# Kernel optimization log

Hardware: AMD Instinct MI355X
Metric: run time of the kernel (lower is better)

Reference implementation:

```python
import jax, jax.numpy as jnp
import numpy as np

L, B, F, H, C = 1024, 8, 256, 8, 32  # seq, batch, feature_dim, heads, head_size
EPS = 1e-5


def setup_inputs() -> dict:
    key = jax.random.key(0)
    ks = jax.random.split(key, 12)
    s = 0.02
    f32 = jnp.float32
    return {
        "features": jax.random.normal(ks[0], (L, B, F), f32),
        "ln_g": jnp.ones((F,), f32),
        "ln_b": jnp.zeros((F,), f32),
        "Wq": jax.random.normal(ks[1], (F, H * C), f32) * s,
        "bq": jnp.zeros((H * C,), f32),
        "Wk": jax.random.normal(ks[2], (F, H * C), f32) * s,
        "bk": jnp.zeros((H * C,), f32),
        "Wv": jax.random.normal(ks[3], (F, H * C), f32) * s,
        "bv": jnp.zeros((H * C,), f32),
        "Wb": jax.random.normal(ks[4], (F, H), f32) * s,
        "bb": jnp.zeros((H,), f32),
        "Wg": jax.random.normal(ks[5], (F, H * C), f32) * s,
        "bg": jnp.zeros((H * C,), f32),
        "Wo": jax.random.normal(ks[6], (H * C, F), f32) * s,
        "bo": jnp.zeros((F,), f32),
    }


def _layernorm(x, g, b):
    mu = jnp.mean(x, axis=-1, keepdims=True)
    var = jnp.var(x, axis=-1, keepdims=True)
    return (x - mu) * jax.lax.rsqrt(var + EPS) * g + b


def reference(features, ln_g, ln_b, Wq, bq, Wk, bk, Wv, bv, Wb, bb, Wg, bg, Wo, bo):
    # features: (L, B, F) -- sequence-first layout (see einsum axis analysis)
    x = _layernorm(features, ln_g, ln_b)
    q = (x @ Wq + bq).reshape(L, B, H, C)  # (Lq, B, H, C)
    k = (x @ Wk + bk).reshape(L, B, H, C)  # (Lk, B, H, C)
    v = (x @ Wv + bv).reshape(L, B, H, C)
    bias = x @ Wb + bb                      # (Lk, B, H) per-key-position bias
    gate = jax.nn.sigmoid(x @ Wg + bg).reshape(L, B, H, C)

    sq_c = 1.0 / np.sqrt(C).astype(np.float32)
    # logits[q, b, k, h]
    logits = jnp.einsum('qbhc,kbhc->qbkh', q, k) * sq_c
    logits = logits + jnp.transpose(bias, (1, 0, 2))[None]  # (1, B, Lk, H)
    w = jax.nn.softmax(logits, axis=2)                      # softmax over keys
    attn = jnp.einsum('qbkh,kbhc->qbhc', w, v)              # (Lq, B, H, C)
    out = (attn * gate).reshape(L, B, H * C)
    return out @ Wo + bo                                    # (L, B, F)
```

## Files before the change

kernel.cpp:

```cpp
#include <hip/hip_runtime.h>
#include <math.h>

#define LQ 1024
#define BB 8
#define FF 256
#define HH 8
#define CC 32
#define MROWS (LQ*BB)
static constexpr float EPSV  = 1e-5f;
static constexpr float LOG2E = 1.4426950408889634f;
static constexpr float C1    = 0.17677669529663687f * 1.4426950408889634f;

typedef short  short8  __attribute__((ext_vector_type(8)));
typedef short  short4v __attribute__((ext_vector_type(4)));
typedef float  float4v __attribute__((ext_vector_type(4)));

__device__ inline unsigned short f2bf(float f) {
    unsigned int u = __builtin_bit_cast(unsigned int, f);
    u += 0x7FFFu + ((u >> 16) & 1u);
    return (unsigned short)(u >> 16);
}
__device__ inline float bf2f(unsigned short h) {
    unsigned int u = ((unsigned int)h) << 16;
    return __builtin_bit_cast(float, u);
}
__device__ inline unsigned int cvt_pk_bf16(float a, float b) {
    unsigned int r;
    asm("v_cvt_pk_bf16_f32 %0, %1, %2" : "=v"(r) : "v"(a), "v"(b));
    return r;
}
__device__ __forceinline__ void gl_lds16(const unsigned short* g, unsigned short* l) {
    __builtin_amdgcn_global_load_lds(
        (const __attribute__((address_space(1))) void*)g,
        (__attribute__((address_space(3))) void*)l, 16, 0, 0);
}

__global__ __launch_bounds__(256)
void prep_ln_kernel(const float* __restrict__ x, const float* __restrict__ g,
                    const float* __restrict__ bln,
                    const float* __restrict__ Wq, const float* __restrict__ Wk,
                    const float* __restrict__ Wv, const float* __restrict__ Wg,
                    const float* __restrict__ Wo, const float* __restrict__ Wb,
                    const float* __restrict__ bq, const float* __restrict__ bk,
                    const float* __restrict__ bv, const float* __restrict__ bg,
                    unsigned short* __restrict__ xb, unsigned short* __restrict__ wt,
                    unsigned short* __restrict__ wto,
                    float* __restrict__ bcomb, float* __restrict__ wbt) {
    int bid = blockIdx.x;
    if (bid < 2048) {
        int wid  = threadIdx.x >> 6;
        int lane = threadIdx.x & 63;
        int row  = bid * 4 + wid;
        float4 v = reinterpret_cast<const float4*>(x + (size_t)row * FF)[lane];
        float s  = v.x + v.y + v.z + v.w;
        float sq = v.x*v.x + v.y*v.y + v.z*v.z + v.w*v.w;
        #pragma unroll
        for (int m = 1; m < 64; m <<= 1) {
            s  += __shfl_xor(s,  m);
            sq += __shfl_xor(sq, m);
        }
        float mean = s * (1.0f / FF);
        float var  = sq * (1.0f / FF) - mean * mean;
        float rstd = rsqrtf(var + EPSV);
        float4 gg = reinterpret_cast<const float4*>(g)[lane];
        float4 bv4 = reinterpret_cast<const float4*>(bln)[lane];
        short4v o;
        o[0] = (short)f2bf((v.x - mean) * rstd * gg.x + bv4.x);
        o[1] = (short)f2bf((v.y - mean) * rstd * gg.y + bv4.y);
        o[2] = (short)f2bf((v.z - mean) * rstd * gg.z + bv4.z);
        o[3] = (short)f2bf((v.w - mean) * rstd * gg.w + bv4.w);
        *reinterpret_cast<short4v*>(xb + (size_t)row * FF + lane * 4) = o;
    } else if (bid < 2112) {
        int k0 = (bid - 2048) * 4;
        int nl = threadIdx.x;
        const float* Ws[5] = {Wq, Wk, Wv, Wg, Wo};
        #pragma unroll
        for (int sel = 0; sel < 5; ++sel) {
            const float* W = Ws[sel];
            short4v o;
            #pragma unroll
            for (int j = 0; j < 4; ++j)
                o[j] = (short)f2bf(W[(size_t)(k0 + j) * 256 + nl]);
            unsigned short* dst = (sel < 4)
                ? (wt + ((size_t)sel * 256 + nl) * 256 + k0)
                : (wto + (size_t)nl * 256 + k0);
            *reinterpret_cast<short4v*>(dst) = o;
        }
        if (k0 == 0) {
            bcomb[nl]       = bq[nl];
            bcomb[256 + nl] = bk[nl];
            bcomb[512 + nl] = bv[nl];
            bcomb[768 + nl] = bg[nl];
        }
    } else {
        int nl = threadIdx.x;
        #pragma unroll
        for (int hh = 0; hh < 8; ++hh)
            wbt[hh * 256 + nl] = Wb[(size_t)nl * 8 + hh];
    }
}

__global__ __launch_bounds__(256)
void qkvg_fused_kernel(const unsigned short* __restrict__ A,
                       const unsigned short* __restrict__ Bt,
                       const float* __restrict__ bcomb,
                       const float* __restrict__ wbt,
                       const float* __restrict__ bbv,
                       unsigned short* __restrict__ outq,
                       float* __restrict__ outb) {
    __shared__ unsigned short Asb[128 * 64];
    __shared__ unsigned short Bsb[128 * 64];
    int bid = blockIdx.x;
    int tid = threadIdx.x;

    if (bid >= 512) {
        int idx = (bid - 512) * 256 + tid;
        int row = idx >> 3, hh = idx & 7;
        const unsigned short* xr = A + (size_t)row * 256;
        const float* wr = wbt + hh * 256;
        float s = 0.f;
        #pragma unroll 4
        for (int i = 0; i < 32; ++i) {
            short8 x8 = *reinterpret_cast<const short8*>(xr + i * 8);
            float4 wa = *reinterpret_cast<const float4*>(wr + i * 8);
            float4 wb2 = *reinterpret_cast<const float4*>(wr + i * 8 + 4);
            s += bf2f((unsigned short)x8[0]) * wa.x + bf2f((unsigned short)x8[1]) * wa.y
               + bf2f((unsigned short)x8[2]) * wa.z + bf2f((unsigned short)x8[3]) * wa.w;
            s += bf2f((unsigned short)x8[4]) * wb2.x + bf2f((unsigned short)x8[5]) * wb2.y
               + bf2f((unsigned short)x8[6]) * wb2.z + bf2f((unsigned short)x8[7]) * wb2.w;
        }
        outb[idx] = s + bbv[hh];
        return;
    }

    int lane = tid & 63;
    int w    = tid >> 6;
    int wm   = w >> 1, wn = w & 1;
    int l15  = lane & 15, lg = lane >> 4;
    int bm   = (bid & 63) * 128;
    int bn   = (bid >> 6) * 128;

    float4v acc[4][4];
    #pragma unroll
    for (int i = 0; i < 4; ++i)
        #pragma unroll
        for (int j = 0; j < 4; ++j)
            acc[i][j] = (float4v){0.f, 0.f, 0.f, 0.f};

    for (int k0 = 0; k0 < 256; k0 += 64) {
        __syncthreads();
        #pragma unroll
        for (int j = 0; j < 4; ++j) {
            int c = w * 4 + j;
            int u = c * 64 + lane;
            int row = u >> 3, slot = u & 7;
            size_t gsw = (size_t)row * 256 + k0 + ((slot ^ (row & 7)) * 8);
            gl_lds16(A + (size_t)bm * 256 + gsw, Asb + c * 512);
            gl_lds16(Bt + (size_t)bn * 256 + gsw, Bsb + c * 512);
        }
        __syncthreads();
        #pragma unroll
        for (int kh = 0; kh < 2; ++kh) {
            int slot = kh * 4 + lg;
            short8 af[4], bf[4];
            #pragma unroll
            for (int mf = 0; mf < 4; ++mf) {
                int row = wm * 64 + mf * 16 + l15;
                af[mf] = *reinterpret_cast<const short8*>(
                    Asb + row * 64 + ((slot ^ (row & 7)) * 8));
            }
            #pragma unroll
            for (int nf = 0; nf < 4; ++nf) {
                int row = wn * 64 + nf * 16 + l15;
                bf[nf] = *reinterpret_cast<const short8*>(
                    Bsb + row * 64 + ((slot ^ (row & 7)) * 8));
            }
            #pragma unroll
            for (int mf = 0; mf < 4; ++mf)
                #pragma unroll
                for (int nf = 0; nf < 4; ++nf)
                    acc[mf][nf] = __builtin_amdgcn_mfma_f32_16x16x32_bf16(
                        bf[nf], af[mf], acc[mf][nf], 0, 0, 0);
        }
    }

    int sel = bn >> 8;
    unsigned short* outp = outq + (size_t)sel * MROWS * 256;
    #pragma unroll
    for (int mf = 0; mf < 4; ++mf) {
        int m = bm + wm * 64 + mf * 16 + l15;
        #pragma unroll
        for (int nf = 0; nf < 4; ++nf) {
            int nglob = bn + wn * 64 + nf * 16 + lg * 4;
            float4 b4 = *reinterpret_cast<const float4*>(bcomb + nglob);
            float v0 = acc[mf][nf][0] + b4.x;
            float v1 = acc[mf][nf][1] + b4.y;
            float v2 = acc[mf][nf][2] + b4.z;
            float v3 = acc[mf][nf][3] + b4.w;
            if (sel == 3) {
                v0 = 1.0f / (1.0f + __expf(-v0));
                v1 = 1.0f / (1.0f + __expf(-v1));
                v2 = 1.0f / (1.0f + __expf(-v2));
                v3 = 1.0f / (1.0f + __expf(-v3));
            }
            uint2 st;
            st.x = cvt_pk_bf16(v0, v1);
            st.y = cvt_pk_bf16(v2, v3);
            *reinterpret_cast<uint2*>(outp + (size_t)m * 256 + (nglob & 255)) = st;
        }
    }
}

__global__ __launch_bounds__(512)
void attn_mfma_kernel(const unsigned short* __restrict__ qkvg,
                      const float* __restrict__ biasp,
                      unsigned short* __restrict__ ag) {
    __shared__ unsigned short ksl[128][40];
    __shared__ unsigned short vt[32 * 128];
    __shared__ unsigned short ps[8][32 * 64];
    __shared__ float bias_s[128];
    const unsigned short* qb = qkvg;
    const unsigned short* kb = qkvg + (size_t)MROWS * 256;
    const unsigned short* vb = qkvg + (size_t)MROWS * 256 * 2;
    const unsigned short* gb = qkvg + (size_t)MROWS * 256 * 3;

    int tid  = threadIdx.x;
    int lane = tid & 63;
    int w    = tid >> 6;
    int l15  = lane & 15, lg = lane >> 4;
    int bh   = blockIdx.y;
    int b    = bh >> 3, h = bh & 7;
    int qg   = w >> 1;
    int kh2  = w & 1;
    int qrow0 = blockIdx.x * 128 + qg * 32;

    int krow = tid >> 2, kc8 = (tid & 3) * 8;
    int cv = (tid & 7) * 4, kp = tid >> 3;

    short8 qf[2];
    #pragma unroll
    for (int qt = 0; qt < 2; ++qt)
        qf[qt] = *reinterpret_cast<const short8*>(
            qb + ((size_t)(qrow0 + qt * 16 + l15) * 8 + b) * 256 + h * 32 + lg * 8);

    float lsum[2] = {0.f, 0.f};
    float4v oacc[2][2];
    #pragma unroll
    for (int i = 0; i < 2; ++i)
        #pragma unroll
        for (int j = 0; j < 2; ++j) oacc[i][j] = (float4v){0.f, 0.f, 0.f, 0.f};

    short8 kreg; short4v v0r, v1r; float breg = 0.f;
    {
        kreg = *reinterpret_cast<const short8*>(
            kb + ((size_t)krow * 8 + b) * 256 + h * 32 + kc8);
        const unsigned short* vp =
            vb + ((size_t)(2 * kp) * 8 + b) * 256 + h * 32 + cv;
        v0r = *reinterpret_cast<const short4v*>(vp);
        v1r = *reinterpret_cast<const short4v*>(vp + 8 * 256);
        if (tid < 128) breg = biasp[(size_t)tid * 64 + b * 8 + h] * LOG2E;
    }

    for (int c0 = 0; c0 < LQ; c0 += 128) {
        __syncthreads();
        *reinterpret_cast<short8*>(&ksl[krow][kc8]) = kreg;
        #pragma unroll
        for (int j = 0; j < 4; ++j) {
            int c = cv + j;
            unsigned int pk = (unsigned int)(unsigned short)v0r[j] |
                              ((unsigned int)(unsigned short)v1r[j] << 16);
            int slot = kp >> 2;
            int off  = c * 128 + ((slot ^ (c & 7)) * 8) + ((2 * kp) & 7);
            *reinterpret_cast<unsigned int*>(&vt[off]) = pk;
        }
        if (tid < 128) bias_s[tid] = breg;
        __syncthreads();
        int cn = c0 + 128;
        if (cn < LQ) {
            kreg = *reinterpret_cast<const short8*>(
                kb + ((size_t)(cn + krow) * 8 + b) * 256 + h * 32 + kc8);
            const unsigned short* vp =
                vb + ((size_t)(cn + 2 * kp) * 8 + b) * 256 + h * 32 + cv;
            v0r = *reinterpret_cast<const short4v*>(vp);
            v1r = *reinterpret_cast<const short4v*>(vp + 8 * 256);
            if (tid < 128) breg = biasp[(size_t)(cn + tid) * 64 + b * 8 + h] * LOG2E;
        }

        __builtin_amdgcn_s_setprio(1);
        float4v sc[2][4];
        #pragma unroll
        for (int kt = 0; kt < 4; ++kt) {
            short8 kf = *reinterpret_cast<const short8*>(
                &ksl[kh2 * 64 + kt * 16 + l15][lg * 8]);
            #pragma unroll
            for (int qt = 0; qt < 2; ++qt)
                sc[qt][kt] = __builtin_amdgcn_mfma_f32_16x16x32_bf16(
                    kf, qf[qt], (float4v){0.f, 0.f, 0.f, 0.f}, 0, 0, 0);
        }
        __builtin_amdgcn_s_setprio(0);

        #pragma unroll
        for (int qt = 0; qt < 2; ++qt) {
            int prow = qt * 16 + l15;
            unsigned short* pw = &ps[w][prow * 64];
            int rsw = prow & 7;
            float psum = 0.f;
            #pragma unroll
            for (int kt = 0; kt < 4; ++kt) {
                float4v b4 = *reinterpret_cast<const float4v*>(
                    &bias_s[kh2 * 64 + kt * 16 + lg * 4]);
                float p0 = __builtin_amdgcn_exp2f(fmaf(sc[qt][kt][0], C1, b4[0]));
                float p1 = __builtin_amdgcn_exp2f(fmaf(sc[qt][kt][1], C1, b4[1]));
                float p2 = __builtin_amdgcn_exp2f(fmaf(sc[qt][kt][2], C1, b4[2]));
                float p3 = __builtin_amdgcn_exp2f(fmaf(sc[qt][kt][3], C1, b4[3]));
                psum += (p0 + p1) + (p2 + p3);
                uint2 pk;
                pk.x = cvt_pk_bf16(p0, p1);
                pk.y = cvt_pk_bf16(p2, p3);
                int slot = kt * 2 + (lg >> 1);
                *reinterpret_cast<uint2*>(
                    &pw[((slot ^ rsw) * 8) + (lg & 1) * 4]) = pk;
            }
            psum += __shfl_xor(psum, 16);
            psum += __shfl_xor(psum, 32);
            lsum[qt] += psum;
        }

        __builtin_amdgcn_s_setprio(1);
        #pragma unroll
        for (int kh = 0; kh < 2; ++kh) {
            int pslot = kh * 4 + lg;
            int vslot = kh2 * 8 + kh * 4 + lg;
            short8 pf[2], vf[2];
            #pragma unroll
            for (int qt = 0; qt < 2; ++qt) {
                int prow = qt * 16 + l15;
                pf[qt] = *reinterpret_cast<const short8*>(
                    &ps[w][prow * 64 + ((pslot ^ (prow & 7)) * 8)]);
            }
            #pragma unroll
            for (int ct = 0; ct < 2; ++ct) {
                int crow = ct * 16 + l15;
                vf[ct] = *reinterpret_cast<const short8*>(
                    &vt[crow * 128 + ((vslot ^ (crow & 7)) * 8)]);
            }
            #pragma unroll
            for (int qt = 0; qt < 2; ++qt)
                #pragma unroll
                for (int ct = 0; ct < 2; ++ct)
                    oacc[qt][ct] = __builtin_amdgcn_mfma_f32_16x16x32_bf16(
                        vf[ct], pf[qt], oacc[qt][ct], 0, 0, 0);
        }
        __builtin_amdgcn_s_setprio(0);
    }

    __syncthreads();
    float* scr = reinterpret_cast<float*>(&ps[0][0]);
    if (kh2) {
        float* dst = scr + ((size_t)(qg * 64 + lane)) * 18;
        #pragma unroll
        for (int qt = 0; qt < 2; ++qt)
            #pragma unroll
            for (int ct = 0; ct < 2; ++ct)
                #pragma unroll
                for (int r = 0; r < 4; ++r)
                    dst[(qt * 2 + ct) * 4 + r] = oacc[qt][ct][r];
        dst[16] = lsum[0];
        dst[17] = lsum[1];
    }
    __syncthreads();
    if (!kh2) {
        const float* src = scr + ((size_t)(qg * 64 + lane)) * 18;
        #pragma unroll
        for (int qt = 0; qt < 2; ++qt)
            #pragma unroll
            for (int ct = 0; ct < 2; ++ct)
                #pragma unroll
                for (int r = 0; r < 4; ++r)
                    oacc[qt][ct][r] += src[(qt * 2 + ct) * 4 + r];
        lsum[0] += src[16];
        lsum[1] += src[17];

        #pragma unroll
        for (int qt = 0; qt < 2; ++qt) {
            float linv = 1.0f / lsum[qt];
            size_t base = ((size_t)(qrow0 + qt * 16 + l15) * 8 + b) * 256 + h * 32;
            #pragma unroll
            for (int ct = 0; ct < 2; ++ct) {
                int cc0 = ct * 16 + lg * 4;
                short4v g4 = *reinterpret_cast<const short4v*>(gb + base + cc0);
                float v0 = oacc[qt][ct][0] * linv * bf2f((unsigned short)g4[0]);
                float v1 = oacc[qt][ct][1] * linv * bf2f((unsigned short)g4[1]);
                float v2 = oacc[qt][ct][2] * linv * bf2f((unsigned short)g4[2]);
                float v3 = oacc[qt][ct][3] * linv * bf2f((unsigned short)g4[3]);
                uint2 st;
                st.x = cvt_pk_bf16(v0, v1);
                st.y = cvt_pk_bf16(v2, v3);
                *reinterpret_cast<uint2*>(ag + base + cc0) = st;
            }
        }
    }
}

__global__ __launch_bounds__(256)
void gemm_out_kernel(const unsigned short* __restrict__ A,
                     const unsigned short* __restrict__ Bt,
                     const float* __restrict__ bias,
                     float* __restrict__ Cout) {
    __shared__ unsigned short Asb[64 * 64];
    __shared__ unsigned short Bsb[64 * 64];
    int tid  = threadIdx.x;
    int lane = tid & 63;
    int w    = tid >> 6;
    int l15  = lane & 15, lg = lane >> 4;
    int bm   = blockIdx.x * 64;
    int bn   = blockIdx.y * 64;

    float4v acc[4];
    #pragma unroll
    for (int i = 0; i < 4; ++i) acc[i] = (float4v){0.f, 0.f, 0.f, 0.f};

    for (int k0 = 0; k0 < 256; k0 += 64) {
        __syncthreads();
        #pragma unroll
        for (int j = 0; j < 2; ++j) {
            int c = w * 2 + j;
            int u = c * 64 + lane;
            int row = u >> 3, slot = u & 7;
            gl_lds16(A + (size_t)(bm + row) * 256 + k0 + ((slot ^ (row & 7)) * 8),
                     Asb + c * 512);
        }
        #pragma unroll
        for (int j = 0; j < 2; ++j) {
            int c = w * 2 + j;
            int u = c * 64 + lane;
            int row = u >> 3, slot = u & 7;
            gl_lds16(Bt + (size_t)(bn + row) * 256 + k0 + ((slot ^ (row & 7)) * 8),
                     Bsb + c * 512);
        }
        __syncthreads();
        #pragma unroll
        for (int kh = 0; kh < 2; ++kh) {
            int slot = kh * 4 + lg;
            short8 af[4], bf;
            #pragma unroll
            for (int mf = 0; mf < 4; ++mf) {
                int row = mf * 16 + l15;
                af[mf] = *reinterpret_cast<const short8*>(
                    Asb + row * 64 + ((slot ^ (row & 7)) * 8));
            }
            {
                int row = w * 16 + l15;
                bf = *reinterpret_cast<const short8*>(
                    Bsb + row * 64 + ((slot ^ (row & 7)) * 8));
            }
            #pragma unroll
            for (int mf = 0; mf < 4; ++mf)
                acc[mf] = __builtin_amdgcn_mfma_f32_16x16x32_bf16(
                    bf, af[mf], acc[mf], 0, 0, 0);
        }
    }
    int c0 = bn + w * 16 + lg * 4;
    float4 b4 = *reinterpret_cast<const float4*>(bias + c0);
    #pragma unroll
    for (int mf = 0; mf < 4; ++mf) {
        int m = bm + mf * 16 + l15;
        float4 o;
        o.x = acc[mf][0] + b4.x;
        o.y = acc[mf][1] + b4.y;
        o.z = acc[mf][2] + b4.z;
        o.w = acc[mf][3] + b4.w;
        *reinterpret_cast<float4*>(Cout + (size_t)m * 256 + c0) = o;
    }
}

extern "C" void kernel_launch(void* const* d_in, const int* in_sizes, int n_in,
                              void* d_out, int out_size, void* d_ws, size_t ws_size,
                              hipStream_t stream) {
    (void)in_sizes; (void)n_in; (void)out_size; (void)ws_size;
    const float* features = (const float*)d_in[0];
    const float* ln_g = (const float*)d_in[1];
    const float* ln_b = (const float*)d_in[2];
    const float* Wq = (const float*)d_in[3];
    const float* bq = (const float*)d_in[4];
    const float* Wk = (const float*)d_in[5];
    const float* bk = (const float*)d_in[6];
    const float* Wv = (const float*)d_in[7];
    const float* bv = (const float*)d_in[8];
    const float* Wb = (const float*)d_in[9];
    const float* bbv = (const float*)d_in[10];
    const float* Wg = (const float*)d_in[11];
    const float* bg = (const float*)d_in[12];
    const float* Wo = (const float*)d_in[13];
    const float* bo = (const float*)d_in[14];
    float* out = (float*)d_out;

    char* wsb = (char*)d_ws;
    unsigned short* xb    = (unsigned short*)(wsb);
    unsigned short* wt    = (unsigned short*)(wsb + 4194304);
    unsigned short* wto   = (unsigned short*)(wsb + 4718592);
    float*          bcomb = (float*)(wsb + 4849664);
    float*          wbt   = (float*)(wsb + 4853760);
    unsigned short* qkvg  = (unsigned short*)(wsb + 4861952);
    float*          biasb = (float*)(wsb + 21639168);
    unsigned short* agb   = (unsigned short*)(wsb + 21901312);

    prep_ln_kernel<<<dim3(2113), dim3(256), 0, stream>>>(
        features, ln_g, ln_b, Wq, Wk, Wv, Wg, Wo, Wb,
        bq, bk, bv, bg, xb, wt, wto, bcomb, wbt);
    qkvg_fused_kernel<<<dim3(768), dim3(256), 0, stream>>>(
        xb, wt, bcomb, wbt, bbv, qkvg, biasb);
    attn_mfma_kernel<<<dim3(8, 64), dim3(512), 0, stream>>>(
        qkvg, biasb, agb);
    gemm_out_kernel<<<dim3(128, 4), dim3(256), 0, stream>>>(
        agb, wto, bo, out);
}
```

Baseline: 58.49 us.

## Double-buffer K/V/bias tiles in LDS to drop one barrier per chunk

The attention kernel now keeps two LDS buffers for the K tile, the transposed V tile and the bias. The next chunk is written into the alternate buffer after the current chunk's compute, which leaves one __syncthreads per iteration instead of two. The LOG2E scaling of the bias moves into the bias-projection kernel so the attention loads no longer multiply. LDS use grows by roughly 18 KB per block, which could lower occupancy.

```diff
diff --git a/kernel.cpp b/kernel.cpp
--- a/kernel.cpp
+++ b/kernel.cpp
@@ -129,7 +129,7 @@
             s += bf2f((unsigned short)x8[4]) * wb2.x + bf2f((unsigned short)x8[5]) * wb2.y
                + bf2f((unsigned short)x8[6]) * wb2.z + bf2f((unsigned short)x8[7]) * wb2.w;
         }
-        outb[idx] = s + bbv[hh];
+        outb[idx] = (s + bbv[hh]) * LOG2E;
         return;
     }
 
@@ -215,10 +215,10 @@
 void attn_mfma_kernel(const unsigned short* __restrict__ qkvg,
                       const float* __restrict__ biasp,
                       unsigned short* __restrict__ ag) {
-    __shared__ unsigned short ksl[128][40];
-    __shared__ unsigned short vt[32 * 128];
+    __shared__ unsigned short ksl[2][128][40];
+    __shared__ unsigned short vt[2][32 * 128];
     __shared__ unsigned short ps[8][32 * 64];
-    __shared__ float bias_s[128];
+    __shared__ float bias_s[2][128];
     const unsigned short* qb = qkvg;
     const unsigned short* kb = qkvg + (size_t)MROWS * 256;
     const unsigned short* vb = qkvg + (size_t)MROWS * 256 * 2;
@@ -258,12 +258,9 @@
             vb + ((size_t)(2 * kp) * 8 + b) * 256 + h * 32 + cv;
         v0r = *reinterpret_cast<const short4v*>(vp);
         v1r = *reinterpret_cast<const short4v*>(vp + 8 * 256);
-        if (tid < 128) breg = biasp[(size_t)tid * 64 + b * 8 + h] * LOG2E;
-    }
-
-    for (int c0 = 0; c0 < LQ; c0 += 128) {
-        __syncthreads();
-        *reinterpret_cast<short8*>(&ksl[krow][kc8]) = kreg;
+        if (tid < 128) breg = biasp[(size_t)tid * 64 + b * 8 + h];
+
+        *reinterpret_cast<short8*>(&ksl[0][krow][kc8]) = kreg;
         #pragma unroll
         for (int j = 0; j < 4; ++j) {
             int c = cv + j;
@@ -271,19 +268,24 @@
                               ((unsigned int)(unsigned short)v1r[j] << 16);
             int slot = kp >> 2;
             int off  = c * 128 + ((slot ^ (c & 7)) * 8) + ((2 * kp) & 7);
-            *reinterpret_cast<unsigned int*>(&vt[off]) = pk;
-        }
-        if (tid < 128) bias_s[tid] = breg;
+            *reinterpret_cast<unsigned int*>(&vt[0][off]) = pk;
+        }
+        if (tid < 128) bias_s[0][tid] = breg;
         __syncthreads();
-        int cn = c0 + 128;
-        if (cn < LQ) {
+    }
+
+    for (int ci = 0; ci < 8; ++ci) {
+        int cur = ci & 1;
+        int cn  = (ci + 1) * 128;
+        bool more = cn < LQ;
+        if (more) {
             kreg = *reinterpret_cast<const short8*>(
                 kb + ((size_t)(cn + krow) * 8 + b) * 256 + h * 32 + kc8);
             const unsigned short* vp =
                 vb + ((size_t)(cn + 2 * kp) * 8 + b) * 256 + h * 32 + cv;
             v0r = *reinterpret_cast<const short4v*>(vp);
             v1r = *reinterpret_cast<const short4v*>(vp + 8 * 256);
-            if (tid < 128) breg = biasp[(size_t)(cn + tid) * 64 + b * 8 + h] * LOG2E;
+            if (tid < 128) breg = biasp[(size_t)(cn + tid) * 64 + b * 8 + h];
         }
 
         __builtin_amdgcn_s_setprio(1);
@@ -291,7 +293,7 @@
         #pragma unroll
         for (int kt = 0; kt < 4; ++kt) {
             short8 kf = *reinterpret_cast<const short8*>(
-                &ksl[kh2 * 64 + kt * 16 + l15][lg * 8]);
+                &ksl[cur][kh2 * 64 + kt * 16 + l15][lg * 8]);
             #pragma unroll
             for (int qt = 0; qt < 2; ++qt)
                 sc[qt][kt] = __builtin_amdgcn_mfma_f32_16x16x32_bf16(
@@ -308,7 +310,7 @@
             #pragma unroll
             for (int kt = 0; kt < 4; ++kt) {
                 float4v b4 = *reinterpret_cast<const float4v*>(
-                    &bias_s[kh2 * 64 + kt * 16 + lg * 4]);
+                    &bias_s[cur][kh2 * 64 + kt * 16 + lg * 4]);
                 float p0 = __builtin_amdgcn_exp2f(fmaf(sc[qt][kt][0], C1, b4[0]));
                 float p1 = __builtin_amdgcn_exp2f(fmaf(sc[qt][kt][1], C1, b4[1]));
                 float p2 = __builtin_amdgcn_exp2f(fmaf(sc[qt][kt][2], C1, b4[2]));
@@ -342,7 +344,7 @@
             for (int ct = 0; ct < 2; ++ct) {
                 int crow = ct * 16 + l15;
                 vf[ct] = *reinterpret_cast<const short8*>(
-                    &vt[crow * 128 + ((vslot ^ (crow & 7)) * 8)]);
+                    &vt[cur][crow * 128 + ((vslot ^ (crow & 7)) * 8)]);
             }
             #pragma unroll
             for (int qt = 0; qt < 2; ++qt)
@@ -352,9 +354,24 @@
                         vf[ct], pf[qt], oacc[qt][ct], 0, 0, 0);
         }
         __builtin_amdgcn_s_setprio(0);
-    }
-
-    __syncthreads();
+
+        if (more) {
+            int nxt = cur ^ 1;
+            *reinterpret_cast<short8*>(&ksl[nxt][krow][kc8]) = kreg;
+            #pragma unroll
+            for (int j = 0; j < 4; ++j) {
+                int c = cv + j;
+                unsigned int pk = (unsigned int)(unsigned short)v0r[j] |
+                                  ((unsigned int)(unsigned short)v1r[j] << 16);
+                int slot = kp >> 2;
+                int off  = c * 128 + ((slot ^ (c & 7)) * 8) + ((2 * kp) & 7);
+                *reinterpret_cast<unsigned int*>(&vt[nxt][off]) = pk;
+            }
+            if (tid < 128) bias_s[nxt][tid] = breg;
+        }
+        __syncthreads();
+    }
+
     float* scr = reinterpret_cast<float*>(&ps[0][0]);
     if (kh2) {
         float* dst = scr + ((size_t)(qg * 64 + lane)) * 18;
```

After: 60.89 us. +4.1%, slower.
